# Optimization experiments

Hardware: AMD Instinct MI355X
Metric: run time of the kernel (lower is better)

The kernel has to match this reference:

```python
import jax, jax.numpy as jnp
import numpy as np

# Each of the 16 binary logic ops (probabilistic relaxation) is affine in (1, a, b, a*b):
# op(a,b) = c0 + ca*a + cb*b + cab*a*b. Rows indexed by op id 0..15.
COEF = jnp.array([
    [0, 0, 0, 0],   # 0: false
    [0, 0, 0, 1],   # 1: a AND b
    [0, 1, 0, -1],  # 2: a AND NOT b
    [0, 1, 0, 0],   # 3: a
    [0, 0, 1, -1],  # 4: NOT a AND b
    [0, 0, 1, 0],   # 5: b
    [0, 1, 1, -2],  # 6: a XOR b
    [0, 1, 1, -1],  # 7: a OR b
    [1, -1, -1, 1], # 8: NOR
    [1, -1, -1, 2], # 9: XNOR
    [1, 0, -1, 0],  # 10: NOT b
    [1, 0, -1, 1],  # 11: a OR NOT b
    [1, -1, 0, 0],  # 12: NOT a
    [1, -1, 0, 1],  # 13: NOT a OR b
    [1, 0, 0, -1],  # 14: NAND
    [1, 0, 0, 0],   # 15: true
], dtype=jnp.float32)

B, C, H, W = 64, 32, 32, 32
K = 64            # num_kernels
D = 4             # tree_depth
S = 2 ** D        # sample_size = 16
RF, STRIDE, PAD = 5, 1, 0


def _make_indices(rng):
    # Replicates get_kernel_indices: per-kernel random (h,w,c) offsets, tiled over all
    # spatial positions. Returns a_idx, b_idx: [K, P, S, 3] with (h, w, c).
    h_starts = np.arange(0, H + 2 * PAD - RF + 1, STRIDE)
    w_starts = np.arange(0, W + 2 * PAD - RF + 1, STRIDE)
    hg, wg = np.meshgrid(h_starts, w_starts, indexing='ij')
    hg, wg = hg.ravel(), wg.ravel()           # [P]
    a_all, b_all = [], []
    for _ in range(K):
        h_off = rng.integers(0, RF, 2 * S)
        w_off = rng.integers(0, RF, 2 * S)
        c_off = rng.integers(0, C, 2 * S)
        hh = h_off[None, :] + hg[:, None]     # [P, 2S]
        ww = w_off[None, :] + wg[:, None]
        cc = np.broadcast_to(c_off[None, :], hh.shape)
        idx = np.stack([hh, ww, cc], axis=-1) # [P, 2S, 3]
        a_all.append(idx[:, :S])
        b_all.append(idx[:, S:])
    return np.stack(a_all).astype(np.int32), np.stack(b_all).astype(np.int32)


def setup_inputs() -> dict:
    key = jax.random.key(0)
    kx, k0, k1, k2, k3, k4 = jax.random.split(key, 6)
    rng = np.random.default_rng(0)
    a_idx, b_idx = _make_indices(rng)
    return {
        'x': jax.random.uniform(kx, (B, C, H, W), dtype=jnp.float32),
        'w0': jax.random.normal(k0, (16, K, 16), dtype=jnp.float32),
        'w1': jax.random.normal(k1, (8, K, 16), dtype=jnp.float32),
        'w2': jax.random.normal(k2, (4, K, 16), dtype=jnp.float32),
        'w3': jax.random.normal(k3, (2, K, 16), dtype=jnp.float32),
        'w4': jax.random.normal(k4, (1, K, 16), dtype=jnp.float32),
        'a_idx': jnp.asarray(a_idx),
        'b_idx': jnp.asarray(b_idx),
    }


def _bin_op(a, b, w):
    # a, b: [B, K, P, L]; w: [L, K, 16] raw logits (softmaxed per original).
    p = jax.nn.softmax(w, axis=-1)                 # [L, K, 16]
    coef = jnp.einsum('lko,oc->ckl', p, COEF)      # [4, K, L]
    c = coef[:, None, :, None, :]                  # [4, 1, K, 1, L]
    return c[0] + c[1] * a + c[2] * b + c[3] * (a * b)


def reference(x, w0, w1, w2, w3, w4, a_idx, b_idx):
    ah, aw, ac = a_idx[..., 0], a_idx[..., 1], a_idx[..., 2]
    bh, bw, bc = b_idx[..., 0], b_idx[..., 1], b_idx[..., 2]
    a = x[:, ac, ah, aw]    # [B, K, P, S]
    b = x[:, bc, bh, bw]
    cur = _bin_op(a, b, w0)
    for w in (w1, w2, w3, w4):
        cur = _bin_op(cur[..., 0::2], cur[..., 1::2], w)
    return cur              # [B, K, P, 1]
```

## Files before the change

kernel.cpp:

```cpp
#include <hip/hip_runtime.h>
#include <hip/hip_bf16.h>


#define B_  64
#define C_  32
#define H_  32
#define W_  32
#define K_  64
#define P_  784
#define CHW (C_*H_*W_)
#define HW  (H_*W_)
#define SITES (K_*P_)
#define NPAIR (P_/2)
#define NQUAD (P_/4)

__constant__ float COEF_[16][4] = {
    {0, 0, 0, 0}, {0, 0, 0, 1}, {0, 1, 0, -1}, {0, 1, 0, 0},
    {0, 0, 1, -1}, {0, 0, 1, 0}, {0, 1, 1, -2}, {0, 1, 1, -1},
    {1, -1, -1, 1}, {1, -1, -1, 2}, {1, 0, -1, 0}, {1, 0, -1, 1},
    {1, -1, 0, 0}, {1, -1, 0, 1}, {1, 0, 0, -1}, {1, 0, 0, 0}
};

typedef float f4a __attribute__((ext_vector_type(4), aligned(4)));

__global__ __launch_bounds__(256) void prep_kernel(
    const int* __restrict__ a_idx, const int* __restrict__ b_idx,
    const float* __restrict__ w0, const float* __restrict__ w1,
    const float* __restrict__ w2, const float* __restrict__ w3,
    const float* __restrict__ w4,
    int* __restrict__ baseAB,
    float4* __restrict__ cws)
{
    const int t = blockIdx.x * 256 + threadIdx.x;
    if (t < K_ * 32) {
        const int k = t >> 5;
        const int j = t & 31;
        const int* src = (j < 16) ? a_idx : b_idx;
        const int l = j & 15;
        const size_t ii = ((size_t)k * P_ * 16 + l) * 3;
        const int h = src[ii + 0];
        const int w = src[ii + 1];
        const int c = src[ii + 2];
        baseAB[t] = (c << 12) + (h << 7) + (w << 2);
    } else if (t < K_ * 32 + K_ * 31) {
        const int tt = t - K_ * 32;
        const int k = tt / 31;
        const int node = tt - k * 31;
        int d, l;
        if      (node < 16) { d = 0; l = node; }
        else if (node < 24) { d = 1; l = node - 16; }
        else if (node < 28) { d = 2; l = node - 24; }
        else if (node < 30) { d = 3; l = node - 28; }
        else                { d = 4; l = 0; }
        const float* W;
        switch (d) {
            case 0: W = w0; break;
            case 1: W = w1; break;
            case 2: W = w2; break;
            case 3: W = w3; break;
            default: W = w4; break;
        }
        const float* row = W + ((size_t)l * K_ + k) * 16;
        float m = row[0];
        #pragma unroll
        for (int o = 1; o < 16; ++o) m = fmaxf(m, row[o]);
        float e[16];
        float Z = 0.0f;
        #pragma unroll
        for (int o = 0; o < 16; ++o) { e[o] = expf(row[o] - m); Z += e[o]; }
        const float inv = 1.0f / Z;
        float c0 = 0.f, c1 = 0.f, c2 = 0.f, c3 = 0.f;
        #pragma unroll
        for (int o = 0; o < 16; ++o) {
            c0 += e[o] * COEF_[o][0];
            c1 += e[o] * COEF_[o][1];
            c2 += e[o] * COEF_[o][2];
            c3 += e[o] * COEF_[o][3];
        }
        cws[tt] = make_float4(c0 * inv, c1 * inv, c2 * inv, c3 * inv);
    }
}

__device__ __forceinline__ float binop(float a, float b, float4 c) {
    return fmaf(b, fmaf(c.w, a, c.z), fmaf(c.y, a, c.x));
}

__global__ __launch_bounds__(1024, 4) void logicconv_main(
    const float* __restrict__ x,
    const int* __restrict__ baseAB,
    const float4* __restrict__ cws,
    float* __restrict__ out)
{
    __shared__ float simg[CHW];

    const int tid = threadIdx.x;
    const int kg  = blockIdx.x >> 5;
    const int bp  = blockIdx.x & 31;
    const int b0  = bp * 2;

    {
        const float4* xi = (const float4*)(x + (size_t)b0 * CHW);
        float4* si = (float4*)simg;
        #pragma unroll
        for (int j = 0; j < 8; ++j)
            si[tid + j * 1024] = xi[tid + j * 1024];
    }
    __syncthreads();

    const int w    = __builtin_amdgcn_readfirstlane(tid >> 6);
    const int lane = tid & 63;
    const int isOdd = (w >> 2) & 1;
    const int kloc  = (w & 3) | ((w >> 3) << 2);
    const int k     = kg * 8 + kloc;

    const int*    __restrict__ bA = baseAB + k * 32;
    const float4* __restrict__ cw = cws + (size_t)k * 31;

    if (!isOdd) {
        const char* sb = (const char*)simg;
        float* __restrict__ o0 = out + ((size_t)b0 * K_ + k) * P_;
        for (int s = 0; s < 7; ++s) {
            const int t = s * 64 + lane;
            if (t < NPAIR) {
                const unsigned row  = (unsigned)t / 14u;
                const unsigned disp = 8u * (unsigned)t + 16u * row;

                float2 y1[8];
                #pragma unroll
                for (int q = 0; q < 2; ++q) {
                    float ev[32];
                    #pragma unroll
                    for (int j = 0; j < 8; ++j) {
                        const int l = q * 8 + j;
                        const unsigned la = (unsigned)bA[l]      + disp;
                        const unsigned lb = (unsigned)bA[16 + l] + disp;
                        ev[4*j+0] = *(const float*)(sb + la);
                        ev[4*j+1] = *(const float*)(sb + la + 4);
                        ev[4*j+2] = *(const float*)(sb + lb);
                        ev[4*j+3] = *(const float*)(sb + lb + 4);
                    }
                    #pragma unroll
                    for (int j = 0; j < 4; ++j) {
                        const int l0 = q * 8 + 2 * j;
                        const int n  = q * 4 + j;
                        const float4 cA = cw[l0], cB = cw[l0 + 1];
                        const float4 cL = cw[16 + n];
                        const float z0x = binop(ev[8*j+0], ev[8*j+2], cA);
                        const float z0y = binop(ev[8*j+1], ev[8*j+3], cA);
                        const float z1x = binop(ev[8*j+4], ev[8*j+6], cB);
                        const float z1y = binop(ev[8*j+5], ev[8*j+7], cB);
                        y1[n].x = binop(z0x, z1x, cL);
                        y1[n].y = binop(z0y, z1y, cL);
                    }
                }
                float2 y2[4];
                #pragma unroll
                for (int l = 0; l < 4; ++l) {
                    const float4 c = cw[24 + l];
                    y2[l].x = binop(y1[2*l].x, y1[2*l+1].x, c);
                    y2[l].y = binop(y1[2*l].y, y1[2*l+1].y, c);
                }
                float2 y3[2];
                #pragma unroll
                for (int l = 0; l < 2; ++l) {
                    const float4 c = cw[28 + l];
                    y3[l].x = binop(y2[2*l].x, y2[2*l+1].x, c);
                    y3[l].y = binop(y2[2*l].y, y2[2*l+1].y, c);
                }
                const float4 c4 = cw[30];
                float2 re;
                re.x = binop(y3[0].x, y3[1].x, c4);
                re.y = binop(y3[0].y, y3[1].y, c4);
                *(float2*)(o0 + 2 * t) = re;
            }
        }
    } else {
        const char* x1 = (const char*)(x + (size_t)(b0 + 1) * CHW);
        float* __restrict__ o1 = out + ((size_t)(b0 + 1) * K_ + k) * P_;
        for (int s = 0; s < 4; ++s) {
            const int t = s * 64 + lane;
            if (t < NQUAD) {
                const unsigned row  = (unsigned)t / 7u;
                const unsigned disp = 16u * (unsigned)t + 16u * row;

                f4a y1[8];
                #pragma unroll
                for (int q = 0; q < 4; ++q) {
                    f4a v[8];
                    #pragma unroll
                    for (int j = 0; j < 4; ++j) {
                        const int l = q * 4 + j;
                        v[2*j]   = *(const f4a*)(x1 + ((unsigned)bA[l]      + disp));
                        v[2*j+1] = *(const f4a*)(x1 + ((unsigned)bA[16 + l] + disp));
                    }
                    #pragma unroll
                    for (int j = 0; j < 2; ++j) {
                        const int l0 = q * 4 + 2 * j;
                        const int n  = q * 2 + j;
                        const float4 cA = cw[l0], cB = cw[l0 + 1];
                        const float4 cL = cw[16 + n];
                        f4a z0, z1;
                        #pragma unroll
                        for (int e = 0; e < 4; ++e) {
                            z0[e] = binop(v[4*j    ][e], v[4*j + 1][e], cA);
                            z1[e] = binop(v[4*j + 2][e], v[4*j + 3][e], cB);
                        }
                        #pragma unroll
                        for (int e = 0; e < 4; ++e)
                            y1[n][e] = binop(z0[e], z1[e], cL);
                    }
                }
                f4a y2[4];
                #pragma unroll
                for (int l = 0; l < 4; ++l) {
                    const float4 c = cw[24 + l];
                    #pragma unroll
                    for (int e = 0; e < 4; ++e)
                        y2[l][e] = binop(y1[2*l][e], y1[2*l+1][e], c);
                }
                f4a y3[2];
                #pragma unroll
                for (int l = 0; l < 2; ++l) {
                    const float4 c = cw[28 + l];
                    #pragma unroll
                    for (int e = 0; e < 4; ++e)
                        y3[l][e] = binop(y2[2*l][e], y2[2*l+1][e], c);
                }
                const float4 c4 = cw[30];
                float4 ro;
                ro.x = binop(y3[0][0], y3[1][0], c4);
                ro.y = binop(y3[0][1], y3[1][1], c4);
                ro.z = binop(y3[0][2], y3[1][2], c4);
                ro.w = binop(y3[0][3], y3[1][3], c4);
                *(float4*)(o1 + 4 * t) = ro;
            }
        }
    }
}

extern "C" void kernel_launch(void* const* d_in, const int* in_sizes, int n_in,
                              void* d_out, int out_size, void* d_ws, size_t ws_size,
                              hipStream_t stream) {
    const float* x     = (const float*)d_in[0];
    const float* w0    = (const float*)d_in[1];
    const float* w1    = (const float*)d_in[2];
    const float* w2    = (const float*)d_in[3];
    const float* w3    = (const float*)d_in[4];
    const float* w4    = (const float*)d_in[5];
    const int*   a_idx = (const int*)d_in[6];
    const int*   b_idx = (const int*)d_in[7];
    float* out = (float*)d_out;

    int*    baseAB = (int*)d_ws;
    float4* cws    = (float4*)((char*)d_ws + (size_t)K_ * 32 * 4);

    prep_kernel<<<16, 256, 0, stream>>>(a_idx, b_idx, w0, w1, w2, w3, w4,
                                        baseAB, cws);

    logicconv_main<<<256, 1024, 0, stream>>>(x, baseAB, cws, out);
}
```

Before: 28.51 us.

## Split output rows in halves per block with an 18-row shared-memory halo tile

Each block now handles half of the output rows (14 of 28), staging only an 18-row slice of the even image into LDS (72KB instead of 128KB) and launching 512 blocks instead of 256. A separate LDS index table is precomputed with a channel stride of 18 rows. The odd-image wavefronts switch from float4 quads to float2 pairs over the half range. The aim is more blocks and less LDS staging per block, which should raise occupancy and parallelism. The cost is redundant halo loads, since the 4 overlapping rows are loaded by both halves.

```diff
diff --git a/kernel.cpp b/kernel.cpp
--- a/kernel.cpp
+++ b/kernel.cpp
@@ -11,8 +11,9 @@
 #define CHW (C_*H_*W_)
 #define HW  (H_*W_)
 #define SITES (K_*P_)
-#define NPAIR (P_/2)
-#define NQUAD (P_/4)
+#define NPAIRH 196
+#define NROWS 18
+#define TILEF (C_*NROWS*W_)
 
 __constant__ float COEF_[16][4] = {
     {0, 0, 0, 0}, {0, 0, 0, 1}, {0, 1, 0, -1}, {0, 1, 0, 0},
@@ -21,14 +22,15 @@
     {1, -1, 0, 0}, {1, -1, 0, 1}, {1, 0, 0, -1}, {1, 0, 0, 0}
 };
 
-typedef float f4a __attribute__((ext_vector_type(4), aligned(4)));
+typedef float f2u __attribute__((ext_vector_type(2), aligned(4)));
 
 __global__ __launch_bounds__(256) void prep_kernel(
     const int* __restrict__ a_idx, const int* __restrict__ b_idx,
     const float* __restrict__ w0, const float* __restrict__ w1,
     const float* __restrict__ w2, const float* __restrict__ w3,
     const float* __restrict__ w4,
-    int* __restrict__ baseAB,
+    int* __restrict__ baseG,
+    int* __restrict__ baseL,
     float4* __restrict__ cws)
 {
     const int t = blockIdx.x * 256 + threadIdx.x;
@@ -41,7 +43,8 @@
         const int h = src[ii + 0];
         const int w = src[ii + 1];
         const int c = src[ii + 2];
-        baseAB[t] = (c << 12) + (h << 7) + (w << 2);
+        baseG[t] = (c << 12) + (h << 7) + (w << 2);
+        baseL[t] = c * 2304 + (h << 7) + (w << 2);
     } else if (t < K_ * 32 + K_ * 31) {
         const int tt = t - K_ * 32;
         const int k = tt / 31;
@@ -85,25 +88,35 @@
     return fmaf(b, fmaf(c.w, a, c.z), fmaf(c.y, a, c.x));
 }
 
-__global__ __launch_bounds__(1024, 4) void logicconv_main(
+__global__ __launch_bounds__(1024) void logicconv_main(
     const float* __restrict__ x,
-    const int* __restrict__ baseAB,
+    const int* __restrict__ baseG,
+    const int* __restrict__ baseL,
     const float4* __restrict__ cws,
     float* __restrict__ out)
 {
-    __shared__ float simg[CHW];
+    __shared__ float simg[TILEF];
 
     const int tid = threadIdx.x;
-    const int kg  = blockIdx.x >> 5;
-    const int bp  = blockIdx.x & 31;
+    const int bid = blockIdx.x;
+    const int bp  = bid & 31;
+    const int ph  = (bid >> 5) & 1;
+    const int kg  = bid >> 6;
     const int b0  = bp * 2;
+    const int rlo = 14 * ph;
 
     {
-        const float4* xi = (const float4*)(x + (size_t)b0 * CHW);
+        const float4* xi = (const float4*)(x + (size_t)b0 * CHW + rlo * W_);
         float4* si = (float4*)simg;
         #pragma unroll
-        for (int j = 0; j < 8; ++j)
-            si[tid + j * 1024] = xi[tid + j * 1024];
+        for (int it = 0; it < 5; ++it) {
+            const int u = it * 1024 + tid;
+            if (u < 4608) {
+                const int c = u / 144;
+                const int j = u - c * 144;
+                si[u] = xi[c * 256 + j];
+            }
+        }
     }
     __syncthreads();
 
@@ -113,36 +126,34 @@
     const int kloc  = (w & 3) | ((w >> 3) << 2);
     const int k     = kg * 8 + kloc;
 
-    const int*    __restrict__ bA = baseAB + k * 32;
     const float4* __restrict__ cw = cws + (size_t)k * 31;
 
     if (!isOdd) {
+        const int* __restrict__ bL = baseL + k * 32;
         const char* sb = (const char*)simg;
-        float* __restrict__ o0 = out + ((size_t)b0 * K_ + k) * P_;
-        for (int s = 0; s < 7; ++s) {
+        float* __restrict__ o0 = out + ((size_t)b0 * K_ + k) * P_ + 392 * ph;
+        for (int s = 0; s < 4; ++s) {
             const int t = s * 64 + lane;
-            if (t < NPAIR) {
-                const unsigned row  = (unsigned)t / 14u;
-                const unsigned disp = 8u * (unsigned)t + 16u * row;
-
+            if (t < NPAIRH) {
+                const unsigned disp = 8u * (unsigned)t + 16u * ((unsigned)t / 14u);
                 float2 y1[8];
                 #pragma unroll
-                for (int q = 0; q < 2; ++q) {
-                    float ev[32];
-                    #pragma unroll
-                    for (int j = 0; j < 8; ++j) {
-                        const int l = q * 8 + j;
-                        const unsigned la = (unsigned)bA[l]      + disp;
-                        const unsigned lb = (unsigned)bA[16 + l] + disp;
+                for (int q = 0; q < 4; ++q) {
+                    float ev[16];
+                    #pragma unroll
+                    for (int j = 0; j < 4; ++j) {
+                        const int l = q * 4 + j;
+                        const unsigned la = (unsigned)bL[l]      + disp;
+                        const unsigned lb = (unsigned)bL[16 + l] + disp;
                         ev[4*j+0] = *(const float*)(sb + la);
                         ev[4*j+1] = *(const float*)(sb + la + 4);
                         ev[4*j+2] = *(const float*)(sb + lb);
                         ev[4*j+3] = *(const float*)(sb + lb + 4);
                     }
                     #pragma unroll
-                    for (int j = 0; j < 4; ++j) {
-                        const int l0 = q * 8 + 2 * j;
-                        const int n  = q * 4 + j;
+                    for (int j = 0; j < 2; ++j) {
+                        const int l0 = q * 4 + 2 * j;
+                        const int n  = q * 2 + j;
                         const float4 cA = cw[l0], cB = cw[l0 + 1];
                         const float4 cL = cw[16 + n];
                         const float z0x = binop(ev[8*j+0], ev[8*j+2], cA);
@@ -175,23 +186,26 @@
             }
         }
     } else {
-        const char* x1 = (const char*)(x + (size_t)(b0 + 1) * CHW);
-        float* __restrict__ o1 = out + ((size_t)(b0 + 1) * K_ + k) * P_;
+        const int* __restrict__ bG = baseG + k * 32;
+        const char* x1 = (const char*)(x + (size_t)(b0 + 1) * CHW) + 1792 * ph;
+        float* __restrict__ o1 = out + ((size_t)(b0 + 1) * K_ + k) * P_ + 392 * ph;
         for (int s = 0; s < 4; ++s) {
             const int t = s * 64 + lane;
-            if (t < NQUAD) {
-                const unsigned row  = (unsigned)t / 7u;
-                const unsigned disp = 16u * (unsigned)t + 16u * row;
-
-                f4a y1[8];
+            if (t < NPAIRH) {
+                const unsigned disp = 8u * (unsigned)t + 16u * ((unsigned)t / 14u);
+                float2 y1[8];
                 #pragma unroll
                 for (int q = 0; q < 4; ++q) {
-                    f4a v[8];
+                    float od[16];
                     #pragma unroll
                     for (int j = 0; j < 4; ++j) {
                         const int l = q * 4 + j;
-                        v[2*j]   = *(const f4a*)(x1 + ((unsigned)bA[l]      + disp));
-                        v[2*j+1] = *(const f4a*)(x1 + ((unsigned)bA[16 + l] + disp));
+                        const f2u va = *(const f2u*)(x1 + ((unsigned)bG[l]      + disp));
+                        const f2u vb = *(const f2u*)(x1 + ((unsigned)bG[16 + l] + disp));
+                        od[4*j+0] = va.x;
+                        od[4*j+1] = va.y;
+                        od[4*j+2] = vb.x;
+                        od[4*j+3] = vb.y;
                     }
                     #pragma unroll
                     for (int j = 0; j < 2; ++j) {
@@ -199,40 +213,33 @@
                         const int n  = q * 2 + j;
                         const float4 cA = cw[l0], cB = cw[l0 + 1];
                         const float4 cL = cw[16 + n];
-                        f4a z0, z1;
-                        #pragma unroll
-                        for (int e = 0; e < 4; ++e) {
-                            z0[e] = binop(v[4*j    ][e], v[4*j + 1][e], cA);
-                            z1[e] = binop(v[4*j + 2][e], v[4*j + 3][e], cB);
-                        }
-                        #pragma unroll
-                        for (int e = 0; e < 4; ++e)
-                            y1[n][e] = binop(z0[e], z1[e], cL);
-                    }
-                }
-                f4a y2[4];
+                        const float z0x = binop(od[8*j+0], od[8*j+2], cA);
+                        const float z0y = binop(od[8*j+1], od[8*j+3], cA);
+                        const float z1x = binop(od[8*j+4], od[8*j+6], cB);
+                        const float z1y = binop(od[8*j+5], od[8*j+7], cB);
+                        y1[n].x = binop(z0x, z1x, cL);
+                        y1[n].y = binop(z0y, z1y, cL);
+                    }
+                }
+                float2 y2[4];
                 #pragma unroll
                 for (int l = 0; l < 4; ++l) {
                     const float4 c = cw[24 + l];
-                    #pragma unroll
-                    for (int e = 0; e < 4; ++e)
-                        y2[l][e] = binop(y1[2*l][e], y1[2*l+1][e], c);
-                }
-                f4a y3[2];
+                    y2[l].x = binop(y1[2*l].x, y1[2*l+1].x, c);
+                    y2[l].y = binop(y1[2*l].y, y1[2*l+1].y, c);
+                }
+                float2 y3[2];
                 #pragma unroll
                 for (int l = 0; l < 2; ++l) {
                     const float4 c = cw[28 + l];
-                    #pragma unroll
-                    for (int e = 0; e < 4; ++e)
-                        y3[l][e] = binop(y2[2*l][e], y2[2*l+1][e], c);
+                    y3[l].x = binop(y2[2*l].x, y2[2*l+1].x, c);
+                    y3[l].y = binop(y2[2*l].y, y2[2*l+1].y, c);
                 }
                 const float4 c4 = cw[30];
-                float4 ro;
-                ro.x = binop(y3[0][0], y3[1][0], c4);
-                ro.y = binop(y3[0][1], y3[1][1], c4);
-                ro.z = binop(y3[0][2], y3[1][2], c4);
-                ro.w = binop(y3[0][3], y3[1][3], c4);
-                *(float4*)(o1 + 4 * t) = ro;
+                float2 ro;
+                ro.x = binop(y3[0].x, y3[1].x, c4);
+                ro.y = binop(y3[0].y, y3[1].y, c4);
+                *(float2*)(o1 + 2 * t) = ro;
             }
         }
     }
@@ -251,11 +258,12 @@
     const int*   b_idx = (const int*)d_in[7];
     float* out = (float*)d_out;
 
-    int*    baseAB = (int*)d_ws;
-    float4* cws    = (float4*)((char*)d_ws + (size_t)K_ * 32 * 4);
+    int*    baseG = (int*)d_ws;
+    int*    baseL = baseG + K_ * 32;
+    float4* cws   = (float4*)(baseL + K_ * 32);
 
     prep_kernel<<<16, 256, 0, stream>>>(a_idx, b_idx, w0, w1, w2, w3, w4,
-                                        baseAB, cws);
-
-    logicconv_main<<<256, 1024, 0, stream>>>(x, baseAB, cws, out);
-}
+                                        baseG, baseL, cws);
+
+    logicconv_main<<<512, 1024, 0, stream>>>(x, baseG, baseL, cws, out);
+}
```

Measured after the change: 37.43 us. 31.3% more time.

## Drop shared-memory image staging; gather directly from global via L2

Applied to the files above, without the earlier changes.

Before, the even half of each block's waves gathered from an image staged in LDS and the odd half read global memory directly. Now every wave reads global memory with float4 gathers, each thread producing four outputs, and the LDS copy and its barrier are removed. The launch changes from 256 blocks of 1024 threads to 1024 blocks of 256 threads, each wave handling one (batch, kernel) pair. This cuts the LDS fill and synchronisation cost and frees occupancy, but all gathers now depend on L1/L2 hit rates instead of LDS bandwidth.

```diff
diff --git a/kernel.cpp b/kernel.cpp
--- a/kernel.cpp
+++ b/kernel.cpp
@@ -11,7 +11,6 @@
 #define CHW (C_*H_*W_)
 #define HW  (H_*W_)
 #define SITES (K_*P_)
-#define NPAIR (P_/2)
 #define NQUAD (P_/4)
 
 __constant__ float COEF_[16][4] = {
@@ -85,155 +84,82 @@
     return fmaf(b, fmaf(c.w, a, c.z), fmaf(c.y, a, c.x));
 }
 
-__global__ __launch_bounds__(1024, 4) void logicconv_main(
+__global__ __launch_bounds__(256) void logicconv_main(
     const float* __restrict__ x,
     const int* __restrict__ baseAB,
     const float4* __restrict__ cws,
     float* __restrict__ out)
 {
-    __shared__ float simg[CHW];
-
     const int tid = threadIdx.x;
-    const int kg  = blockIdx.x >> 5;
+    const int kt  = blockIdx.x >> 5;
     const int bp  = blockIdx.x & 31;
-    const int b0  = bp * 2;
-
-    {
-        const float4* xi = (const float4*)(x + (size_t)b0 * CHW);
-        float4* si = (float4*)simg;
-        #pragma unroll
-        for (int j = 0; j < 8; ++j)
-            si[tid + j * 1024] = xi[tid + j * 1024];
-    }
-    __syncthreads();
 
     const int w    = __builtin_amdgcn_readfirstlane(tid >> 6);
     const int lane = tid & 63;
-    const int isOdd = (w >> 2) & 1;
-    const int kloc  = (w & 3) | ((w >> 3) << 2);
-    const int k     = kg * 8 + kloc;
+    const int k    = kt * 2 + (w & 1);
+    const int b    = bp * 2 + (w >> 1);
 
     const int*    __restrict__ bA = baseAB + k * 32;
     const float4* __restrict__ cw = cws + (size_t)k * 31;
+    const char* xb = (const char*)(x + (size_t)b * CHW);
+    float* __restrict__ ob = out + ((size_t)b * K_ + k) * P_;
 
-    if (!isOdd) {
-        const char* sb = (const char*)simg;
-        float* __restrict__ o0 = out + ((size_t)b0 * K_ + k) * P_;
-        for (int s = 0; s < 7; ++s) {
-            const int t = s * 64 + lane;
-            if (t < NPAIR) {
-                const unsigned row  = (unsigned)t / 14u;
-                const unsigned disp = 8u * (unsigned)t + 16u * row;
+    for (int s = 0; s < 4; ++s) {
+        const int t = s * 64 + lane;
+        if (t < NQUAD) {
+            const unsigned row  = (unsigned)t / 7u;
+            const unsigned disp = 16u * (unsigned)t + 16u * row;
 
-                float2 y1[8];
+            f4a y1[8];
+            #pragma unroll
+            for (int q = 0; q < 4; ++q) {
+                f4a v[8];
                 #pragma unroll
-                for (int q = 0; q < 2; ++q) {
-                    float ev[32];
+                for (int j = 0; j < 4; ++j) {
+                    const int l = q * 4 + j;
+                    v[2*j]   = *(const f4a*)(xb + ((unsigned)bA[l]      + disp));
+                    v[2*j+1] = *(const f4a*)(xb + ((unsigned)bA[16 + l] + disp));
+                }
+                #pragma unroll
+                for (int j = 0; j < 2; ++j) {
+                    const int l0 = q * 4 + 2 * j;
+                    const int n  = q * 2 + j;
+                    const float4 cA = cw[l0], cB = cw[l0 + 1];
+                    const float4 cL = cw[16 + n];
+                    f4a z0, z1;
                     #pragma unroll
-                    for (int j = 0; j < 8; ++j) {
-                        const int l = q * 8 + j;
-                        const unsigned la = (unsigned)bA[l]      + disp;
-                        const unsigned lb = (unsigned)bA[16 + l] + disp;
-                        ev[4*j+0] = *(const float*)(sb + la);
-                        ev[4*j+1] = *(const float*)(sb + la + 4);
-                        ev[4*j+2] = *(const float*)(sb + lb);
-                        ev[4*j+3] = *(const float*)(sb + lb + 4);
+                    for (int e = 0; e < 4; ++e) {
+                        z0[e] = binop(v[4*j    ][e], v[4*j + 1][e], cA);
+                        z1[e] = binop(v[4*j + 2][e], v[4*j + 3][e], cB);
                     }
                     #pragma unroll
-                    for (int j = 0; j < 4; ++j) {
-                        const int l0 = q * 8 + 2 * j;
-                        const int n  = q * 4 + j;
-                        const float4 cA = cw[l0], cB = cw[l0 + 1];
-                        const float4 cL = cw[16 + n];
-                        const float z0x = binop(ev[8*j+0], ev[8*j+2], cA);
-                        const float z0y = binop(ev[8*j+1], ev[8*j+3], cA);
-                        const float z1x = binop(ev[8*j+4], ev[8*j+6], cB);
-                        const float z1y = binop(ev[8*j+5], ev[8*j+7], cB);
-                        y1[n].x = binop(z0x, z1x, cL);
-                        y1[n].y = binop(z0y, z1y, cL);
-                    }
+                    for (int e = 0; e < 4; ++e)
+                        y1[n][e] = binop(z0[e], z1[e], cL);
                 }
-                float2 y2[4];
+            }
+            f4a y2[4];
+            #pragma unroll
+            for (int l = 0; l < 4; ++l) {
+                const float4 c = cw[24 + l];
                 #pragma unroll
-                for (int l = 0; l < 4; ++l) {
-                    const float4 c = cw[24 + l];
-                    y2[l].x = binop(y1[2*l].x, y1[2*l+1].x, c);
-                    y2[l].y = binop(y1[2*l].y, y1[2*l+1].y, c);
-                }
-                float2 y3[2];
+                for (int e = 0; e < 4; ++e)
+                    y2[l][e] = binop(y1[2*l][e], y1[2*l+1][e], c);
+            }
+            f4a y3[2];
+            #pragma unroll
+            for (int l = 0; l < 2; ++l) {
+                const float4 c = cw[28 + l];
                 #pragma unroll
-                for (int l = 0; l < 2; ++l) {
-                    const float4 c = cw[28 + l];
-                    y3[l].x = binop(y2[2*l].x, y2[2*l+1].x, c);
-                    y3[l].y = binop(y2[2*l].y, y2[2*l+1].y, c);
-                }
-                const float4 c4 = cw[30];
-                float2 re;
-                re.x = binop(y3[0].x, y3[1].x, c4);
-                re.y = binop(y3[0].y, y3[1].y, c4);
-                *(float2*)(o0 + 2 * t) = re;
+                for (int e = 0; e < 4; ++e)
+                    y3[l][e] = binop(y2[2*l][e], y2[2*l+1][e], c);
             }
-        }
-    } else {
-        const char* x1 = (const char*)(x + (size_t)(b0 + 1) * CHW);
-        float* __restrict__ o1 = out + ((size_t)(b0 + 1) * K_ + k) * P_;
-        for (int s = 0; s < 4; ++s) {
-            const int t = s * 64 + lane;
-            if (t < NQUAD) {
-                const unsigned row  = (unsigned)t / 7u;
-                const unsigned disp = 16u * (unsigned)t + 16u * row;
-
-                f4a y1[8];
-                #pragma unroll
-                for (int q = 0; q < 4; ++q) {
-                    f4a v[8];
-                    #pragma unroll
-                    for (int j = 0; j < 4; ++j) {
-                        const int l = q * 4 + j;
-                        v[2*j]   = *(const f4a*)(x1 + ((unsigned)bA[l]      + disp));
-                        v[2*j+1] = *(const f4a*)(x1 + ((unsigned)bA[16 + l] + disp));
-                    }
-                    #pragma unroll
-                    for (int j = 0; j < 2; ++j) {
-                        const int l0 = q * 4 + 2 * j;
-                        const int n  = q * 2 + j;
-                        const float4 cA = cw[l0], cB = cw[l0 + 1];
-                        const float4 cL = cw[16 + n];
-                        f4a z0, z1;
-                        #pragma unroll
-                        for (int e = 0; e < 4; ++e) {
-                            z0[e] = binop(v[4*j    ][e], v[4*j + 1][e], cA);
-                            z1[e] = binop(v[4*j + 2][e], v[4*j + 3][e], cB);
-                        }
-                        #pragma unroll
-                        for (int e = 0; e < 4; ++e)
-                            y1[n][e] = binop(z0[e], z1[e], cL);
-                    }
-                }
-                f4a y2[4];
-                #pragma unroll
-                for (int l = 0; l < 4; ++l) {
-                    const float4 c = cw[24 + l];
-                    #pragma unroll
-                    for (int e = 0; e < 4; ++e)
-                        y2[l][e] = binop(y1[2*l][e], y1[2*l+1][e], c);
-                }
-                f4a y3[2];
-                #pragma unroll
-                for (int l = 0; l < 2; ++l) {
-                    const float4 c = cw[28 + l];
-                    #pragma unroll
-                    for (int e = 0; e < 4; ++e)
-                        y3[l][e] = binop(y2[2*l][e], y2[2*l+1][e], c);
-                }
-                const float4 c4 = cw[30];
-                float4 ro;
-                ro.x = binop(y3[0][0], y3[1][0], c4);
-                ro.y = binop(y3[0][1], y3[1][1], c4);
-                ro.z = binop(y3[0][2], y3[1][2], c4);
-                ro.w = binop(y3[0][3], y3[1][3], c4);
-                *(float4*)(o1 + 4 * t) = ro;
-            }
+            const float4 c4 = cw[30];
+            float4 ro;
+            ro.x = binop(y3[0][0], y3[1][0], c4);
+            ro.y = binop(y3[0][1], y3[1][1], c4);
+            ro.z = binop(y3[0][2], y3[1][2], c4);
+            ro.w = binop(y3[0][3], y3[1][3], c4);
+            *(float4*)(ob + 4 * t) = ro;
         }
     }
 }
@@ -257,5 +183,5 @@
     prep_kernel<<<16, 256, 0, stream>>>(a_idx, b_idx, w0, w1, w2, w3, w4,
                                         baseAB, cws);
 
-    logicconv_main<<<256, 1024, 0, stream>>>(x, baseAB, cws, out);
+    logicconv_main<<<32 * 32, 256, 0, stream>>>(x, baseAB, cws, out);
 }
```

After: 33.15 us. +16.3%, slower.

## Halve LDS image, split positions across waves, double grid size

Applied to the files above, without the earlier changes.

The main kernel now stages only half of the even image (channels 0-15, 64KB) into shared memory and reads the other channels directly from global memory via a per-index branch. Each block covers 4 kernels instead of 8, and each kernel's spatial positions are split between two waves, so the grid doubles to 512 blocks. The block index mapping is also remapped so neighbouring blocks share batch pairs. The goal is to lower LDS footprint and the serial load phase so more blocks can be resident and parallelism improves. The cost is divergent global loads for high channels and redundant image staging across more blocks.

```diff
diff --git a/kernel.cpp b/kernel.cpp
--- a/kernel.cpp
+++ b/kernel.cpp
@@ -21,6 +21,7 @@
     {1, -1, 0, 0}, {1, -1, 0, 1}, {1, 0, 0, -1}, {1, 0, 0, 0}
 };
 
+typedef float f2u __attribute__((ext_vector_type(2), aligned(4)));
 typedef float f4a __attribute__((ext_vector_type(4), aligned(4)));
 
 __global__ __launch_bounds__(256) void prep_kernel(
@@ -85,43 +86,51 @@
     return fmaf(b, fmaf(c.w, a, c.z), fmaf(c.y, a, c.x));
 }
 
-__global__ __launch_bounds__(1024, 4) void logicconv_main(
+__global__ __launch_bounds__(1024) void logicconv_main(
     const float* __restrict__ x,
     const int* __restrict__ baseAB,
     const float4* __restrict__ cws,
     float* __restrict__ out)
 {
-    __shared__ float simg[CHW];
-
-    const int tid = threadIdx.x;
-    const int kg  = blockIdx.x >> 5;
-    const int bp  = blockIdx.x & 31;
-    const int b0  = bp * 2;
+    __shared__ float simg[16384];
+
+    const int tid   = threadIdx.x;
+    const int bid   = blockIdx.x;
+    const int bp_hi = bid >> 6;
+    const int mid   = bid & 63;
+    const int kq    = mid >> 2;
+    const int bp_lo = mid & 3;
+    const int bp    = bp_hi * 4 + bp_lo;
+    const int b0    = bp * 2;
 
     {
         const float4* xi = (const float4*)(x + (size_t)b0 * CHW);
         float4* si = (float4*)simg;
         #pragma unroll
-        for (int j = 0; j < 8; ++j)
+        for (int j = 0; j < 4; ++j)
             si[tid + j * 1024] = xi[tid + j * 1024];
     }
     __syncthreads();
 
-    const int w    = __builtin_amdgcn_readfirstlane(tid >> 6);
-    const int lane = tid & 63;
-    const int isOdd = (w >> 2) & 1;
-    const int kloc  = (w & 3) | ((w >> 3) << 2);
-    const int k     = kg * 8 + kloc;
+    const int w      = __builtin_amdgcn_readfirstlane(tid >> 6);
+    const int lane   = tid & 63;
+    const int isOdd  = (w >> 2) & 1;
+    const int r3     = (w & 3) | ((w >> 3) << 2);
+    const int klocal = r3 >> 1;
+    const int sub    = r3 & 1;
+    const int k      = kq * 4 + klocal;
 
     const int*    __restrict__ bA = baseAB + k * 32;
     const float4* __restrict__ cw = cws + (size_t)k * 31;
 
     if (!isOdd) {
         const char* sb = (const char*)simg;
+        const char* xe = (const char*)(x + (size_t)b0 * CHW);
         float* __restrict__ o0 = out + ((size_t)b0 * K_ + k) * P_;
-        for (int s = 0; s < 7; ++s) {
-            const int t = s * 64 + lane;
-            if (t < NPAIR) {
+        for (int s = 0; s < 4; ++s) {
+            const int tl = s * 64 + lane;
+            if (tl < 196) {
+                const int t = sub * 196 + tl;
                 const unsigned row  = (unsigned)t / 14u;
                 const unsigned disp = 8u * (unsigned)t + 16u * row;
 
@@ -132,12 +141,26 @@
                     #pragma unroll
                     for (int j = 0; j < 8; ++j) {
                         const int l = q * 8 + j;
-                        const unsigned la = (unsigned)bA[l]      + disp;
-                        const unsigned lb = (unsigned)bA[16 + l] + disp;
-                        ev[4*j+0] = *(const float*)(sb + la);
-                        ev[4*j+1] = *(const float*)(sb + la + 4);
-                        ev[4*j+2] = *(const float*)(sb + lb);
-                        ev[4*j+3] = *(const float*)(sb + lb + 4);
+                        const int baA = bA[l];
+                        const int baB = bA[16 + l];
+                        if (baA < 65536) {
+                            const unsigned la = (unsigned)baA + disp;
+                            ev[4*j+0] = *(const float*)(sb + la);
+                            ev[4*j+1] = *(const float*)(sb + la + 4);
+                        } else {
+                            const f2u va = *(const f2u*)(xe + ((unsigned)baA + disp));
+                            ev[4*j+0] = va.x;
+                            ev[4*j+1] = va.y;
+                        }
+                        if (baB < 65536) {
+                            const unsigned lb = (unsigned)baB + disp;
+                            ev[4*j+2] = *(const float*)(sb + lb);
+                            ev[4*j+3] = *(const float*)(sb + lb + 4);
+                        } else {
+                            const f2u vb = *(const f2u*)(xe + ((unsigned)baB + disp));
+                            ev[4*j+2] = vb.x;
+                            ev[4*j+3] = vb.y;
+                        }
                     }
                     #pragma unroll
                     for (int j = 0; j < 4; ++j) {
@@ -177,9 +200,10 @@
     } else {
         const char* x1 = (const char*)(x + (size_t)(b0 + 1) * CHW);
         float* __restrict__ o1 = out + ((size_t)(b0 + 1) * K_ + k) * P_;
-        for (int s = 0; s < 4; ++s) {
-            const int t = s * 64 + lane;
-            if (t < NQUAD) {
+        for (int s = 0; s < 2; ++s) {
+            const int tl = s * 64 + lane;
+            if (tl < 98) {
+                const int t = sub * 98 + tl;
                 const unsigned row  = (unsigned)t / 7u;
                 const unsigned disp = 16u * (unsigned)t + 16u * row;
 
@@ -257,5 +281,5 @@
     prep_kernel<<<16, 256, 0, stream>>>(a_idx, b_idx, w0, w1, w2, w3, w4,
                                         baseAB, cws);
 
-    logicconv_main<<<256, 1024, 0, stream>>>(x, baseAB, cws, out);
-}
+    logicconv_main<<<512, 1024, 0, stream>>>(x, baseAB, cws, out);
+}
```

After: 44.51 us. 56.1% more time.
